# Optimization experiments

Hardware: AMD Instinct MI355X
Metric: run time of the kernel (lower is better)

## Reference

```python
import jax, jax.numpy as jnp
import numpy as np

# constants from init_kwargs (data_info / model_cfg)
FX = 300.0
FY = 300.0
CX = 128.0
CY = 128.0
BG = 1.0            # data_info['bg_color']
EPS2D = 0.3         # gsplat screen-space blur added to 2D covariance diagonal
NEAR = 0.01         # gsplat near-plane cull
C0 = 0.28209479177387814  # SH degree-0 basis
N_PTS = 512
IMG = 256


def quat_to_rotmat(q):
    # q: (N,4) wxyz, normalized inside
    q = q / jnp.linalg.norm(q, axis=-1, keepdims=True)
    w, x, y, z = q[:, 0], q[:, 1], q[:, 2], q[:, 3]
    return jnp.stack([
        jnp.stack([1 - 2 * (y * y + z * z), 2 * (x * y - w * z), 2 * (x * z + w * y)], -1),
        jnp.stack([2 * (x * y + w * z), 1 - 2 * (x * x + z * z), 2 * (y * z - w * x)], -1),
        jnp.stack([2 * (x * z - w * y), 2 * (y * z + w * x), 1 - 2 * (x * x + y * y)], -1),
    ], axis=-2)  # (N,3,3)


def setup_inputs() -> dict:
    key = jax.random.key(0)
    k = jax.random.split(key, 6)
    means = (jax.random.uniform(k[0], (N_PTS, 3), dtype=jnp.float32) - 0.5) * 10.0
    quats = jax.random.normal(k[1], (N_PTS, 4), dtype=jnp.float32)
    # log-scales around 0.2m so Gaussians actually cover pixels
    scales = jnp.log(0.2) + 0.1 * jax.random.normal(k[2], (N_PTS, 3), dtype=jnp.float32)
    opacities = jax.random.normal(k[3], (N_PTS,), dtype=jnp.float32)
    sh0 = 0.5 * jax.random.normal(k[4], (N_PTS, 1, 3), dtype=jnp.float32)
    shN = 0.01 * jax.random.normal(k[5], (N_PTS, 15, 3), dtype=jnp.float32)
    camtoworld = jnp.concatenate([jnp.eye(3, dtype=jnp.float32), jnp.zeros((3, 1), jnp.float32)], axis=1)
    return {"camtoworld": camtoworld, "means": means, "quats": quats, "scales": scales,
            "opacities": opacities, "sh0": sh0, "shN": shN, "img_h": IMG, "img_w": IMG}


def _render(camtoworld, means, quats, scales, opacities, sh0, shN, img_h, img_w):
    # --- camera setup (matches module forward) ---
    c2w = jnp.eye(4, dtype=jnp.float32).at[:3, :].set(camtoworld)
    viewmat = jnp.linalg.inv(c2w)
    viewmat = viewmat.at[1, :].multiply(-1.0).at[2, :].multiply(-1.0)
    R, t = viewmat[:3, :3], viewmat[:3, 3]

    # --- project means ---
    p = means @ R.T + t                      # (N,3) camera-space
    x, y, z = p[:, 0], p[:, 1], p[:, 2]
    valid = z > NEAR
    zs = jnp.where(valid, z, 1.0)
    rz = 1.0 / zs

    # --- 3D covariance: R(q) diag(s^2) R(q)^T, rotated to camera ---
    Rq = quat_to_rotmat(quats)
    M = Rq * jnp.exp(scales)[:, None, :]
    cov3d = M @ jnp.swapaxes(M, 1, 2)        # (N,3,3)
    cov_cam = jnp.einsum('ij,njk,lk->nil', R, cov3d, R)

    # --- EWA perspective Jacobian with fov clipping (gsplat persp_proj) ---
    limx = 1.3 * (0.5 * img_w / FX)
    limy = 1.3 * (0.5 * img_h / FY)
    tx = zs * jnp.clip(x * rz, -limx, limx)
    ty = zs * jnp.clip(y * rz, -limy, limy)
    zero = jnp.zeros_like(rz)
    J = jnp.stack([
        jnp.stack([FX * rz, zero, -FX * tx * rz * rz], -1),
        jnp.stack([zero, FY * rz, -FY * ty * rz * rz], -1),
    ], axis=1)                               # (N,2,3)
    cov2d = jnp.einsum('nij,njk,nlk->nil', J, cov_cam, J)
    a = cov2d[:, 0, 0] + EPS2D
    b = cov2d[:, 0, 1]
    c = cov2d[:, 1, 1] + EPS2D
    det = a * c - b * b
    valid = valid & (det > 1e-12)
    dets = jnp.where(valid, det, 1.0)
    cA, cB, cC = c / dets, -b / dets, a / dets   # conic (inverse 2D covariance)

    mx = FX * x * rz + CX
    my = FY * y * rz + CY

    # --- colors: sh_degree = 0 -> only sh0 band, clamped to >= 0 ---
    color = jnp.maximum(C0 * sh0[:, 0, :] + 0.5, 0.0)   # (N,3)
    opac = jax.nn.sigmoid(opacities)

    # --- depth sort (front to back) ---
    order = jnp.argsort(jnp.where(valid, z, jnp.inf))
    mx, my, cA, cB, cC, opac, color, valid = (v[order] for v in (mx, my, cA, cB, cC, opac, color, valid))

    # --- per-pixel alpha evaluation (dense [N,H,W]) ---
    px = jnp.arange(img_w, dtype=jnp.float32) + 0.5
    py = jnp.arange(img_h, dtype=jnp.float32) + 0.5
    dx = px[None, None, :] - mx[:, None, None]          # (N,H,W)
    dy = py[None, :, None] - my[:, None, None]
    sigma = 0.5 * (cA[:, None, None] * dx * dx + cC[:, None, None] * dy * dy) + cB[:, None, None] * dx * dy
    alpha = jnp.minimum(0.999, opac[:, None, None] * jnp.exp(-sigma))
    alpha = jnp.where((sigma >= 0.0) & (alpha >= 1.0 / 255.0) & valid[:, None, None], alpha, 0.0)

    # --- front-to-back alpha compositing via exclusive cumprod of (1-alpha) ---
    T = jnp.cumprod(1.0 - alpha, axis=0)                # (N,H,W)
    T_excl = jnp.concatenate([jnp.ones_like(T[:1]), T[:-1]], axis=0)
    w = T_excl * alpha
    render = jnp.einsum('nhw,nc->hwc', w, color) + T[-1][..., None] * BG   # (H,W,3)
    alpha_map = (1.0 - T[-1])[..., None]                                   # (H,W,1)
    return render, alpha_map


def reference(camtoworld, means, quats, scales, opacities, sh0, shN, img_h, img_w):
    return _render(camtoworld, means, quats, scales, opacities, sh0, shN, img_h, img_w)
```

## Files before the change

kernel.cpp:

```cpp
#include <hip/hip_runtime.h>
#include <math.h>

#define FXc 300.0f
#define FYc 300.0f
#define CXc 128.0f
#define CYc 128.0f
#define BGc 1.0f
#define EPS2Dc 0.3f
#define NEARc 0.01f
#define C0c 0.28209479177387814f

#define MAXP 512

__global__ void __launch_bounds__(256)
gs_fused(const float* __restrict__ cam,
         const float* __restrict__ means,
         const float* __restrict__ quats,
         const float* __restrict__ scales,
         const float* __restrict__ opacs,
         const float* __restrict__ sh0,
         const int* __restrict__ img_w_p,
         float* __restrict__ out,
         int n, int npix)
{
    __shared__ float4 spts[MAXP][3];
    __shared__ float  zc[MAXP + 4];
    __shared__ int    scnt[MAXP / 64];
    __shared__ int    sbase[MAXP / 64 + 1];

    const int lt   = threadIdx.x;
    const int wave = lt >> 6, lane = lt & 63;

    const int W = *img_w_p;
    const int tiles_x = W >> 4;
    const int tx = (blockIdx.x % tiles_x) << 4;
    const int ty = (blockIdx.x / tiles_x) << 4;
    const int col = tx + (lt & 15);
    const int row = ty + (lt >> 4);
    const float px = (float)col + 0.5f;
    const float py = (float)row + 0.5f;
    const float tx0 = (float)tx + 0.5f, tx1 = (float)tx + 15.5f;
    const float ty0 = (float)ty + 0.5f, ty1 = (float)ty + 15.5f;

    const float a00 = cam[0], a01 = cam[1], a02 = cam[2],  b0 = cam[3];
    const float a10 = cam[4], a11 = cam[5], a12 = cam[6],  b1 = cam[7];
    const float a20 = cam[8], a21 = cam[9], a22 = cam[10], b2 = cam[11];
    const float det3 = a00*(a11*a22 - a12*a21) - a01*(a10*a22 - a12*a20) + a02*(a10*a21 - a11*a20);
    const float id = 1.0f / det3;
    const float i00 = (a11*a22 - a12*a21)*id, i01 = (a02*a21 - a01*a22)*id, i02 = (a01*a12 - a02*a11)*id;
    const float i10 = (a12*a20 - a10*a22)*id, i11 = (a00*a22 - a02*a20)*id, i12 = (a02*a10 - a00*a12)*id;
    const float i20 = (a10*a21 - a11*a20)*id, i21 = (a01*a20 - a00*a21)*id, i22 = (a00*a11 - a01*a10)*id;
    const float R00 = i00,  R01 = i01,  R02 = i02;
    const float R10 = -i10, R11 = -i11, R12 = -i12;
    const float R20 = -i20, R21 = -i21, R22 = -i22;
    const float t0 = -(i00*b0 + i01*b1 + i02*b2);
    const float t1 = (i10*b0 + i11*b1 + i12*b2);
    const float t2 = (i20*b0 + i21*b1 + i22*b2);

    const float limx = 1.3f * (0.5f * 256.0f / FXc) * ((float)W / 256.0f);
    const float limy = limx;
    const float limx_e = 1.3f * (0.5f * (float)W / FXc);
    const float limy_e = limx_e;

    float pmx[2], pmy[2], pA_[2], pB_[2], pC_[2], pop[2], pcr[2], pcg[2], pcb[2], pz[2];
    unsigned long long mreg[2];
    bool phit[2];

    const int nchunks = (n + 63) >> 6;

    for (int r = 0; r < 2; ++r) {
        const int p = (r << 8) + lt;
        bool hit = false;
        float mx = 0.f, my = 0.f, cA = 0.f, cB = 0.f, cC = 0.f;
        float op = 0.f, cr = 0.f, cg = 0.f, cb = 0.f, z = 0.f;

        if (p < n) {
            const float m0 = means[3*p], m1 = means[3*p+1], m2 = means[3*p+2];
            const float px_ = R00*m0 + R01*m1 + R02*m2 + t0;
            const float py_ = R10*m0 + R11*m1 + R12*m2 + t1;
            const float pz_ = R20*m0 + R21*m1 + R22*m2 + t2;

            bool valid = pz_ > NEARc;
            const float zs = valid ? pz_ : 1.0f;
            const float rz = 1.0f / zs;

            float qw = quats[4*p], qx = quats[4*p+1], qy = quats[4*p+2], qz = quats[4*p+3];
            const float qn = rsqrtf(qw*qw + qx*qx + qy*qy + qz*qz);
            qw *= qn; qx *= qn; qy *= qn; qz *= qn;
            const float Rq00 = 1.f - 2.f*(qy*qy + qz*qz), Rq01 = 2.f*(qx*qy - qw*qz), Rq02 = 2.f*(qx*qz + qw*qy);
            const float Rq10 = 2.f*(qx*qy + qw*qz), Rq11 = 1.f - 2.f*(qx*qx + qz*qz), Rq12 = 2.f*(qy*qz - qw*qx);
            const float Rq20 = 2.f*(qx*qz - qw*qy), Rq21 = 2.f*(qy*qz + qw*qx), Rq22 = 1.f - 2.f*(qx*qx + qy*qy);

            const float e0 = __expf(scales[3*p]), e1 = __expf(scales[3*p+1]), e2 = __expf(scales[3*p+2]);
            const float M00 = Rq00*e0, M01 = Rq01*e1, M02 = Rq02*e2;
            const float M10 = Rq10*e0, M11 = Rq11*e1, M12 = Rq12*e2;
            const float M20 = Rq20*e0, M21 = Rq21*e1, M22 = Rq22*e2;

            const float S00 = M00*M00 + M01*M01 + M02*M02;
            const float S01 = M00*M10 + M01*M11 + M02*M12;
            const float S02 = M00*M20 + M01*M21 + M02*M22;
            const float S11 = M10*M10 + M11*M11 + M12*M12;
            const float S12 = M10*M20 + M11*M21 + M12*M22;
            const float S22 = M20*M20 + M21*M21 + M22*M22;

            const float U00 = R00*S00 + R01*S01 + R02*S02;
            const float U01 = R00*S01 + R01*S11 + R02*S12;
            const float U02 = R00*S02 + R01*S12 + R02*S22;
            const float U10 = R10*S00 + R11*S01 + R12*S02;
            const float U11 = R10*S01 + R11*S11 + R12*S12;
            const float U12 = R10*S02 + R11*S12 + R12*S22;
            const float U20 = R20*S00 + R21*S01 + R22*S02;
            const float U21 = R20*S01 + R21*S11 + R22*S12;
            const float U22 = R20*S02 + R21*S12 + R22*S22;

            const float C00 = U00*R00 + U01*R01 + U02*R02;
            const float C01 = U00*R10 + U01*R11 + U02*R12;
            const float C02 = U00*R20 + U01*R21 + U02*R22;
            const float C11 = U10*R10 + U11*R11 + U12*R12;
            const float C12 = U10*R20 + U11*R21 + U12*R22;
            const float C22 = U20*R20 + U21*R21 + U22*R22;

            const float txc = zs * fminf(fmaxf(px_*rz, -limx_e), limx_e);
            const float tyc = zs * fminf(fmaxf(py_*rz, -limy_e), limy_e);
            const float ja0 = FXc * rz;
            const float ja2 = -FXc * txc * rz * rz;
            const float jb1 = FYc * rz;
            const float jb2 = -FYc * tyc * rz * rz;

            const float c2d00 = ja0*ja0*C00 + 2.f*ja0*ja2*C02 + ja2*ja2*C22 + EPS2Dc;
            const float c2d01 = ja0*jb1*C01 + ja0*jb2*C02 + ja2*jb1*C12 + ja2*jb2*C22;
            const float c2d11 = jb1*jb1*C11 + 2.f*jb1*jb2*C12 + jb2*jb2*C22 + EPS2Dc;

            const float det2 = c2d00*c2d11 - c2d01*c2d01;
            valid = valid && (det2 > 1e-12f);
            const float rdet = 1.0f / (valid ? det2 : 1.0f);
            cA = c2d11 * rdet;
            cB = -c2d01 * rdet;
            cC = c2d00 * rdet;

            mx = FXc * px_ * rz + CXc;
            my = FYc * py_ * rz + CYc;

            cr = fmaxf(C0c * sh0[3*p+0] + 0.5f, 0.0f);
            cg = fmaxf(C0c * sh0[3*p+1] + 0.5f, 0.0f);
            cb = fmaxf(C0c * sh0[3*p+2] + 0.5f, 0.0f);
            op = 1.0f / (1.0f + __expf(-opacs[p]));
            z  = pz_;

            const float op255 = op * 255.0f;
            if (valid && op255 >= 1.0f) {
                const float s = __logf(op255);
                const float dxm = sqrtf(2.0f * s * c2d00) * 1.0001f + 0.01f;
                const float dym = sqrtf(2.0f * s * c2d11) * 1.0001f + 0.01f;
                hit = (mx - dxm <= tx1) && (mx + dxm >= tx0) &&
                      (my - dym <= ty1) && (my + dym >= ty0);
            }
        }

        mreg[r] = __ballot(hit);
        phit[r] = hit;
        pmx[r] = mx; pmy[r] = my; pA_[r] = cA; pB_[r] = cB; pC_[r] = cC;
        pop[r] = op; pcr[r] = cr; pcg[r] = cg; pcb[r] = cb; pz[r] = z;
        const int c = (r << 2) + wave;
        if (lane == 0 && c < (MAXP/64)) scnt[c] = __popcll(mreg[r]);
    }
    __syncthreads();

    if (lt == 0) {
        int acc = 0;
        for (int c = 0; c < nchunks; ++c) { sbase[c] = acc; acc += scnt[c]; }
        sbase[nchunks] = acc;
    }
    __syncthreads();
    const int k = sbase[nchunks];

    int pslot[2] = {-1, -1};
    for (int r = 0; r < 2; ++r) {
        if (phit[r]) {
            const int c = (r << 2) + wave;
            const int slot = sbase[c] + __popcll(mreg[r] & ((1ull << lane) - 1ull));
            pslot[r] = slot;
            zc[slot] = pz[r];
        }
    }
    if (lt < 4) zc[k + lt] = INFINITY;
    __syncthreads();

    if (pslot[0] >= 0 || pslot[1] >= 0) {
        const float za = pz[0], zb = pz[1];
        const int sa = pslot[0], sb = pslot[1];
        int rank0 = 0, rank1 = 0;
        const float4* z4 = (const float4*)zc;
        const int k4 = (k + 3) >> 2;
        for (int j4 = 0; j4 < k4; ++j4) {
            const float4 v = z4[j4];
            const int j = j4 << 2;
            rank0 += (v.x < za || (v.x == za && (j+0) < sa));
            rank0 += (v.y < za || (v.y == za && (j+1) < sa));
            rank0 += (v.z < za || (v.z == za && (j+2) < sa));
            rank0 += (v.w < za || (v.w == za && (j+3) < sa));
            rank1 += (v.x < zb || (v.x == zb && (j+0) < sb));
            rank1 += (v.y < zb || (v.y == zb && (j+1) < sb));
            rank1 += (v.z < zb || (v.z == zb && (j+2) < sb));
            rank1 += (v.w < zb || (v.w == zb && (j+3) < sb));
        }
        if (sa >= 0) {
            spts[rank0][0] = make_float4(pmx[0], pmy[0], pA_[0], pB_[0]);
            spts[rank0][1] = make_float4(pC_[0], pop[0], pcr[0], pcg[0]);
            spts[rank0][2] = make_float4(pcb[0], 0.f, 0.f, 0.f);
        }
        if (sb >= 0) {
            spts[rank1][0] = make_float4(pmx[1], pmy[1], pA_[1], pB_[1]);
            spts[rank1][1] = make_float4(pC_[1], pop[1], pcr[1], pcg[1]);
            spts[rank1][2] = make_float4(pcb[1], 0.f, 0.f, 0.f);
        }
    }
    __syncthreads();

    float T = 1.0f, r_ = 0.f, g_ = 0.f, b_ = 0.f;
    for (int base = 0; base < k; base += 16) {
        const int lim = (base + 16 < k) ? base + 16 : k;
        #pragma unroll 4
        for (int i = base; i < lim; ++i) {
            const float4 a4 = spts[i][0];
            const float4 b4 = spts[i][1];
            const float  cbv = spts[i][2].x;

            const float dx = px - a4.x;
            const float dy = py - a4.y;
            const float sigma = 0.5f * (a4.z*dx*dx + b4.x*dy*dy) + a4.w*dx*dy;
            float al = b4.y * __expf(-sigma);
            al = fminf(al, 0.999f);
            const bool keep = (sigma >= 0.0f) && (al >= (1.0f/255.0f));
            al = keep ? al : 0.0f;

            const float w = T * al;
            r_ += w * b4.z;
            g_ += w * b4.w;
            b_ += w * cbv;
            T *= (1.0f - al);
        }
        if (!__any(T > 1e-4f)) break;
    }

    r_ += T * BGc; g_ += T * BGc; b_ += T * BGc;

    const int pix = row * W + col;
    if (pix < npix) {
        out[3*pix + 0] = r_;
        out[3*pix + 1] = g_;
        out[3*pix + 2] = b_;
        out[3*npix + pix] = 1.0f - T;
    }
}

extern "C" void kernel_launch(void* const* d_in, const int* in_sizes, int n_in,
                              void* d_out, int out_size, void* d_ws, size_t ws_size,
                              hipStream_t stream) {
    const float* cam    = (const float*)d_in[0];
    const float* means  = (const float*)d_in[1];
    const float* quats  = (const float*)d_in[2];
    const float* scales = (const float*)d_in[3];
    const float* opacs  = (const float*)d_in[4];
    const float* sh0    = (const float*)d_in[5];
    const int* img_w = (const int*)d_in[8];

    const int n = in_sizes[4];
    const int npix = out_size / 4;

    const int blocks = npix / 256;
    gs_fused<<<blocks, 256, 0, stream>>>(cam, means, quats, scales, opacs, sh0,
                                         img_w, (float*)d_out, n, npix);
}
```

Measured before the change: 11.30 us.

## Split per-tile splat list across four depth segments and merge transmittance

Each block now uses 1024 threads. Every point is preprocessed by its own thread instead of two points per thread, and the sorted per-tile splat list is split into four contiguous depth segments, with each 256-thread group compositing one segment for the same 256 pixels. The partial colors and transmittances are merged front-to-back through shared memory. This shortens the serial compositing chain per thread, but it gives up early termination across segments: later segments do their work even if earlier ones are already opaque. It also adds shared memory and a merge barrier.

```diff
diff --git a/kernel.cpp b/kernel.cpp
--- a/kernel.cpp
+++ b/kernel.cpp
@@ -11,8 +11,9 @@
 #define C0c 0.28209479177387814f
 
 #define MAXP 512
-
-__global__ void __launch_bounds__(256)
+#define SEG  4
+
+__global__ void __launch_bounds__(1024)
 gs_fused(const float* __restrict__ cam,
          const float* __restrict__ means,
          const float* __restrict__ quats,
@@ -24,9 +25,10 @@
          int n, int npix)
 {
     __shared__ float4 spts[MAXP][3];
-    __shared__ float  zc[MAXP + 4];
-    __shared__ int    scnt[MAXP / 64];
-    __shared__ int    sbase[MAXP / 64 + 1];
+    __shared__ __align__(16) float zc[MAXP + 4];
+    __shared__ int scnt[MAXP / 64];
+    __shared__ int sbase[MAXP / 64 + 1];
+    __shared__ float4 comb[SEG - 1][256];
 
     const int lt   = threadIdx.x;
     const int wave = lt >> 6, lane = lt & 63;
@@ -35,45 +37,36 @@
     const int tiles_x = W >> 4;
     const int tx = (blockIdx.x % tiles_x) << 4;
     const int ty = (blockIdx.x / tiles_x) << 4;
-    const int col = tx + (lt & 15);
-    const int row = ty + (lt >> 4);
-    const float px = (float)col + 0.5f;
-    const float py = (float)row + 0.5f;
     const float tx0 = (float)tx + 0.5f, tx1 = (float)tx + 15.5f;
     const float ty0 = (float)ty + 0.5f, ty1 = (float)ty + 15.5f;
 
-    const float a00 = cam[0], a01 = cam[1], a02 = cam[2],  b0 = cam[3];
-    const float a10 = cam[4], a11 = cam[5], a12 = cam[6],  b1 = cam[7];
-    const float a20 = cam[8], a21 = cam[9], a22 = cam[10], b2 = cam[11];
-    const float det3 = a00*(a11*a22 - a12*a21) - a01*(a10*a22 - a12*a20) + a02*(a10*a21 - a11*a20);
-    const float id = 1.0f / det3;
-    const float i00 = (a11*a22 - a12*a21)*id, i01 = (a02*a21 - a01*a22)*id, i02 = (a01*a12 - a02*a11)*id;
-    const float i10 = (a12*a20 - a10*a22)*id, i11 = (a00*a22 - a02*a20)*id, i12 = (a02*a10 - a00*a12)*id;
-    const float i20 = (a10*a21 - a11*a20)*id, i21 = (a01*a20 - a00*a21)*id, i22 = (a00*a11 - a01*a10)*id;
-    const float R00 = i00,  R01 = i01,  R02 = i02;
-    const float R10 = -i10, R11 = -i11, R12 = -i12;
-    const float R20 = -i20, R21 = -i21, R22 = -i22;
-    const float t0 = -(i00*b0 + i01*b1 + i02*b2);
-    const float t1 = (i10*b0 + i11*b1 + i12*b2);
-    const float t2 = (i20*b0 + i21*b1 + i22*b2);
-
-    const float limx = 1.3f * (0.5f * 256.0f / FXc) * ((float)W / 256.0f);
-    const float limy = limx;
-    const float limx_e = 1.3f * (0.5f * (float)W / FXc);
-    const float limy_e = limx_e;
-
-    float pmx[2], pmy[2], pA_[2], pB_[2], pC_[2], pop[2], pcr[2], pcg[2], pcb[2], pz[2];
-    unsigned long long mreg[2];
-    bool phit[2];
-
     const int nchunks = (n + 63) >> 6;
 
-    for (int r = 0; r < 2; ++r) {
-        const int p = (r << 8) + lt;
+    float pmx = 0.f, pmy = 0.f, pA_ = 0.f, pB_ = 0.f, pC_ = 0.f;
+    float pop = 0.f, pcr = 0.f, pcg = 0.f, pcb = 0.f, pz = 0.f;
+    unsigned long long mreg = 0ull;
+    bool phit = false;
+
+    if (lt < MAXP) {
+        const float a00 = cam[0], a01 = cam[1], a02 = cam[2],  b0 = cam[3];
+        const float a10 = cam[4], a11 = cam[5], a12 = cam[6],  b1 = cam[7];
+        const float a20 = cam[8], a21 = cam[9], a22 = cam[10], b2 = cam[11];
+        const float det3 = a00*(a11*a22 - a12*a21) - a01*(a10*a22 - a12*a20) + a02*(a10*a21 - a11*a20);
+        const float id = 1.0f / det3;
+        const float i00 = (a11*a22 - a12*a21)*id, i01 = (a02*a21 - a01*a22)*id, i02 = (a01*a12 - a02*a11)*id;
+        const float i10 = (a12*a20 - a10*a22)*id, i11 = (a00*a22 - a02*a20)*id, i12 = (a02*a10 - a00*a12)*id;
+        const float i20 = (a10*a21 - a11*a20)*id, i21 = (a01*a20 - a00*a21)*id, i22 = (a00*a11 - a01*a10)*id;
+        const float R00 = i00,  R01 = i01,  R02 = i02;
+        const float R10 = -i10, R11 = -i11, R12 = -i12;
+        const float R20 = -i20, R21 = -i21, R22 = -i22;
+        const float t0 = -(i00*b0 + i01*b1 + i02*b2);
+        const float t1 = (i10*b0 + i11*b1 + i12*b2);
+        const float t2 = (i20*b0 + i21*b1 + i22*b2);
+        const float limx_e = 1.3f * (0.5f * (float)W / FXc);
+        const float limy_e = limx_e;
+
+        const int p = lt;
         bool hit = false;
-        float mx = 0.f, my = 0.f, cA = 0.f, cB = 0.f, cC = 0.f;
-        float op = 0.f, cr = 0.f, cg = 0.f, cb = 0.f, z = 0.f;
-
         if (p < n) {
             const float m0 = means[3*p], m1 = means[3*p+1], m2 = means[3*p+2];
             const float px_ = R00*m0 + R01*m1 + R02*m2 + t0;
@@ -134,35 +127,31 @@
             const float det2 = c2d00*c2d11 - c2d01*c2d01;
             valid = valid && (det2 > 1e-12f);
             const float rdet = 1.0f / (valid ? det2 : 1.0f);
-            cA = c2d11 * rdet;
-            cB = -c2d01 * rdet;
-            cC = c2d00 * rdet;
-
-            mx = FXc * px_ * rz + CXc;
-            my = FYc * py_ * rz + CYc;
-
-            cr = fmaxf(C0c * sh0[3*p+0] + 0.5f, 0.0f);
-            cg = fmaxf(C0c * sh0[3*p+1] + 0.5f, 0.0f);
-            cb = fmaxf(C0c * sh0[3*p+2] + 0.5f, 0.0f);
-            op = 1.0f / (1.0f + __expf(-opacs[p]));
-            z  = pz_;
-
-            const float op255 = op * 255.0f;
+            pA_ = c2d11 * rdet;
+            pB_ = -c2d01 * rdet;
+            pC_ = c2d00 * rdet;
+
+            pmx = FXc * px_ * rz + CXc;
+            pmy = FYc * py_ * rz + CYc;
+
+            pcr = fmaxf(C0c * sh0[3*p+0] + 0.5f, 0.0f);
+            pcg = fmaxf(C0c * sh0[3*p+1] + 0.5f, 0.0f);
+            pcb = fmaxf(C0c * sh0[3*p+2] + 0.5f, 0.0f);
+            pop = 1.0f / (1.0f + __expf(-opacs[p]));
+            pz  = pz_;
+
+            const float op255 = pop * 255.0f;
             if (valid && op255 >= 1.0f) {
                 const float s = __logf(op255);
                 const float dxm = sqrtf(2.0f * s * c2d00) * 1.0001f + 0.01f;
                 const float dym = sqrtf(2.0f * s * c2d11) * 1.0001f + 0.01f;
-                hit = (mx - dxm <= tx1) && (mx + dxm >= tx0) &&
-                      (my - dym <= ty1) && (my + dym >= ty0);
+                hit = (pmx - dxm <= tx1) && (pmx + dxm >= tx0) &&
+                      (pmy - dym <= ty1) && (pmy + dym >= ty0);
             }
         }
-
-        mreg[r] = __ballot(hit);
-        phit[r] = hit;
-        pmx[r] = mx; pmy[r] = my; pA_[r] = cA; pB_[r] = cB; pC_[r] = cC;
-        pop[r] = op; pcr[r] = cr; pcg[r] = cg; pcb[r] = cb; pz[r] = z;
-        const int c = (r << 2) + wave;
-        if (lane == 0 && c < (MAXP/64)) scnt[c] = __popcll(mreg[r]);
+        phit = hit;
+        mreg = __ballot(hit);
+        if (lane == 0) scnt[wave] = __popcll(mreg);
     }
     __syncthreads();
 
@@ -174,52 +163,47 @@
     __syncthreads();
     const int k = sbase[nchunks];
 
-    int pslot[2] = {-1, -1};
-    for (int r = 0; r < 2; ++r) {
-        if (phit[r]) {
-            const int c = (r << 2) + wave;
-            const int slot = sbase[c] + __popcll(mreg[r] & ((1ull << lane) - 1ull));
-            pslot[r] = slot;
-            zc[slot] = pz[r];
-        }
+    int pslot = -1;
+    if (lt < MAXP && phit) {
+        pslot = sbase[wave] + __popcll(mreg & ((1ull << lane) - 1ull));
+        zc[pslot] = pz;
     }
     if (lt < 4) zc[k + lt] = INFINITY;
     __syncthreads();
 
-    if (pslot[0] >= 0 || pslot[1] >= 0) {
-        const float za = pz[0], zb = pz[1];
-        const int sa = pslot[0], sb = pslot[1];
-        int rank0 = 0, rank1 = 0;
+    if (pslot >= 0) {
+        const float za = pz;
+        const int sa = pslot;
+        int rank = 0;
         const float4* z4 = (const float4*)zc;
         const int k4 = (k + 3) >> 2;
         for (int j4 = 0; j4 < k4; ++j4) {
             const float4 v = z4[j4];
             const int j = j4 << 2;
-            rank0 += (v.x < za || (v.x == za && (j+0) < sa));
-            rank0 += (v.y < za || (v.y == za && (j+1) < sa));
-            rank0 += (v.z < za || (v.z == za && (j+2) < sa));
-            rank0 += (v.w < za || (v.w == za && (j+3) < sa));
-            rank1 += (v.x < zb || (v.x == zb && (j+0) < sb));
-            rank1 += (v.y < zb || (v.y == zb && (j+1) < sb));
-            rank1 += (v.z < zb || (v.z == zb && (j+2) < sb));
-            rank1 += (v.w < zb || (v.w == zb && (j+3) < sb));
-        }
-        if (sa >= 0) {
-            spts[rank0][0] = make_float4(pmx[0], pmy[0], pA_[0], pB_[0]);
-            spts[rank0][1] = make_float4(pC_[0], pop[0], pcr[0], pcg[0]);
-            spts[rank0][2] = make_float4(pcb[0], 0.f, 0.f, 0.f);
-        }
-        if (sb >= 0) {
-            spts[rank1][0] = make_float4(pmx[1], pmy[1], pA_[1], pB_[1]);
-            spts[rank1][1] = make_float4(pC_[1], pop[1], pcr[1], pcg[1]);
-            spts[rank1][2] = make_float4(pcb[1], 0.f, 0.f, 0.f);
-        }
-    }
-    __syncthreads();
+            rank += (v.x < za || (v.x == za && (j+0) < sa));
+            rank += (v.y < za || (v.y == za && (j+1) < sa));
+            rank += (v.z < za || (v.z == za && (j+2) < sa));
+            rank += (v.w < za || (v.w == za && (j+3) < sa));
+        }
+        spts[rank][0] = make_float4(pmx, pmy, pA_, pB_);
+        spts[rank][1] = make_float4(pC_, pop, pcr, pcg);
+        spts[rank][2] = make_float4(pcb, 0.f, 0.f, 0.f);
+    }
+    __syncthreads();
+
+    const int s   = lt >> 8;
+    const int pix = lt & 255;
+    const int col = tx + (pix & 15);
+    const int row = ty + (pix >> 4);
+    const float px = (float)col + 0.5f;
+    const float py = (float)row + 0.5f;
+
+    const int beg = (k * s) >> 2;
+    const int end = (k * (s + 1)) >> 2;
 
     float T = 1.0f, r_ = 0.f, g_ = 0.f, b_ = 0.f;
-    for (int base = 0; base < k; base += 16) {
-        const int lim = (base + 16 < k) ? base + 16 : k;
+    for (int base = beg; base < end; base += 16) {
+        const int lim = (base + 16 < end) ? base + 16 : end;
         #pragma unroll 4
         for (int i = base; i < lim; ++i) {
             const float4 a4 = spts[i][0];
@@ -243,14 +227,26 @@
         if (!__any(T > 1e-4f)) break;
     }
 
-    r_ += T * BGc; g_ += T * BGc; b_ += T * BGc;
-
-    const int pix = row * W + col;
-    if (pix < npix) {
-        out[3*pix + 0] = r_;
-        out[3*pix + 1] = g_;
-        out[3*pix + 2] = b_;
-        out[3*npix + pix] = 1.0f - T;
+    if (s > 0) comb[s - 1][pix] = make_float4(r_, g_, b_, T);
+    __syncthreads();
+
+    if (s == 0) {
+        const float4 f1 = comb[0][pix];
+        const float4 f2 = comb[1][pix];
+        const float4 f3 = comb[2][pix];
+        float rr = r_ + T * (f1.x + f1.w * (f2.x + f2.w * f3.x));
+        float gg = g_ + T * (f1.y + f1.w * (f2.y + f2.w * f3.y));
+        float bb = b_ + T * (f1.z + f1.w * (f2.z + f2.w * f3.z));
+        const float Tt = T * f1.w * f2.w * f3.w;
+        rr += Tt * BGc; gg += Tt * BGc; bb += Tt * BGc;
+
+        const int opix = row * W + col;
+        if (opix < npix) {
+            out[3*opix + 0] = rr;
+            out[3*opix + 1] = gg;
+            out[3*opix + 2] = bb;
+            out[3*npix + opix] = 1.0f - Tt;
+        }
     }
 }
 
@@ -269,6 +265,6 @@
     const int npix = out_size / 4;
 
     const int blocks = npix / 256;
-    gs_fused<<<blocks, 256, 0, stream>>>(cam, means, quats, scales, opacs, sh0,
-                                         img_w, (float*)d_out, n, npix);
+    gs_fused<<<blocks, 1024, 0, stream>>>(cam, means, quats, scales, opacs, sh0,
+                                          img_w, (float*)d_out, n, npix);
 }
```

Result: faster. 10.47 us (-7.4%).
